# Kernel tuning notes

Measured on AMD Instinct MI355X. Metric: run time of the kernel, lower is better.

Reference implementation:

```python
import jax, jax.numpy as jnp
import numpy as np

BATCH, MAXPV = 32, 50
RULENUM, PROPNUM = 256, 256  # must be equal (eye(rulenum) * property_importance)
ENT_DIM, RULE_DIM = 128, 128
ENTITYNUM = 50000
THRESHOLD = 0.5


def _l2norm(x, eps=1e-12):
    # F.normalize(p=2, dim=-1)
    n = jnp.linalg.norm(x, axis=-1, keepdims=True)
    return x / jnp.clip(n, eps)


def setup_inputs() -> dict:
    key = jax.random.key(0)
    ks = jax.random.split(key, 20)
    d_in = ENT_DIM + RULE_DIM
    inp = {
        'property': jax.random.randint(ks[0], (BATCH, MAXPV), 0, ENTITYNUM),
        'value': jax.random.randint(ks[1], (BATCH, MAXPV), 0, ENTITYNUM),
        'samemask': jax.random.randint(ks[2], (BATCH, MAXPV), 0, 2),
        'padmask': jax.random.randint(ks[3], (BATCH, MAXPV), 0, 2),
        'rule_embedding': jax.random.normal(ks[4], (RULENUM, RULE_DIM), jnp.float32),
        'entity_table': jax.random.normal(ks[5], (ENTITYNUM, ENT_DIM), jnp.float32),
        # Linear weights stored (in, out); concat order in the original is (p_emb, rule_emb)
        'fc1_w': jax.random.normal(ks[6], (d_in, ENT_DIM), jnp.float32),
        'fc1_b': jax.random.normal(ks[7], (ENT_DIM,), jnp.float32) * 0.02,
        'fc2_w': jax.random.normal(ks[8], (d_in, ENT_DIM), jnp.float32),
        'fc2_b': jax.random.normal(ks[9], (ENT_DIM,), jnp.float32) * 0.02,
        'fc3_w': jax.random.normal(ks[10], (d_in, ENT_DIM), jnp.float32),
        'fc3_b': jax.random.normal(ks[11], (ENT_DIM,), jnp.float32) * 0.02,
        'fc4_w': jax.random.normal(ks[12], (ENT_DIM, 1), jnp.float32) * 0.05,
        'fc4_b': jax.random.normal(ks[13], (1,), jnp.float32) * 0.02,
        'fc5_w': jax.random.normal(ks[14], (ENT_DIM, 1), jnp.float32) * 0.05,
        'fc5_b': jax.random.normal(ks[15], (1,), jnp.float32) * 0.02,
        'fc6_w': jax.random.normal(ks[16], (ENT_DIM, ENT_DIM), jnp.float32) * 0.05,
        'fc6_b': jax.random.normal(ks[17], (ENT_DIM,), jnp.float32) * 0.02,
    }
    return inp


def reference(property, value, samemask, padmask, rule_embedding, entity_table,
              fc1_w, fc1_b, fc2_w, fc2_b, fc3_w, fc3_b,
              fc4_w, fc4_b, fc5_w, fc5_b, fc6_w, fc6_b):
    E = entity_table.shape[1]
    R = rule_embedding.shape[0]
    P = R  # propertynum == rulenum (required by eye() regularizer)

    p_emb = _l2norm(entity_table[property])   # (B, M, E)
    v_emb = _l2norm(entity_table[value])      # (B, M, E)
    r_emb = _l2norm(rule_embedding)           # (R, Dr)

    # cat(p, rule) -> Linear decomposed into two smaller matmuls (same math)
    def branch(w, b):
        return p_emb @ w[:E], r_emb @ w[E:] + b  # (B,M,Eo), (R,Eo)

    # s1 branch
    pa, ra = branch(fc1_w, fc1_b)
    h1 = jax.nn.relu(pa[:, None, :, :] + ra[None, :, None, :])   # (B,R,M,E)
    s1 = jax.nn.sigmoid(h1 @ fc4_w + fc4_b)[..., 0]              # (B,R,M)

    # p branch
    pb, rb = branch(fc2_w, fc2_b)
    h2 = jax.nn.relu(pb[:, None, :, :] + rb[None, :, None, :])
    p = jax.nn.sigmoid(h2 @ fc5_w + fc5_b)[..., 0]               # (B,R,M)

    # s2 branch
    pc, rc = branch(fc3_w, fc3_b)
    h3 = jax.nn.relu(pc[:, None, :, :] + rc[None, :, None, :])
    gv = _l2norm(h3 @ fc6_w + fc6_b)                             # (B,R,M,E)
    vb = v_emb[:, None, :, :]                                    # (B,1,M,E)
    denom = jnp.clip(jnp.linalg.norm(vb, axis=-1) * jnp.linalg.norm(gv, axis=-1), 1e-8)
    cos = jnp.sum(vb * gv, axis=-1) / denom
    s2 = 0.5 * cos + 0.5                                         # (B,R,M)

    score = p + (1.0 - p) * s2
    score = jnp.where(samemask[:, None, :] == 1, s1 * score, 1.0 - s1)

    # property importance K: fc1/fc4 on cat(prop_emb, rule_emb)
    prop_emb = _l2norm(entity_table[:P])                         # propertyids = arange(P)
    pi_h = jax.nn.relu((prop_emb @ fc1_w[:E])[None, :, :]
                       + (r_emb @ fc1_w[E:] + fc1_b)[:, None, :])  # (R,P,E)
    pi = jax.nn.sigmoid(pi_h @ fc4_w + fc4_b)[..., 0]            # (R,P)

    rule_mask = jnp.sum(pi * (pi > THRESHOLD), axis=-1) + 1.0    # (R,)

    score = score * padmask[:, None, :].astype(score.dtype)
    score = score * (s1 > THRESHOLD)
    score = jnp.sum(score, axis=-1) / rule_mask[None, :]          # (B,R)
    pooledscore = jnp.max(score, axis=1)                          # (B,)

    diag = jnp.eye(R, dtype=pi.dtype)
    reg = pi * diag + (1.0 - pi) * (1.0 - diag)
    reg = -jnp.log(reg + 1e-8) * (1.0 - diag + diag * R)
    reg_logits = jnp.mean(reg)
    return pooledscore, reg_logits
```

## Files before the change

kernel.cpp:

```cpp
#include <hip/hip_runtime.h>
#include <hip/hip_bf16.h>

#define BATCH 32
#define MAXPV 50
#define RN 256
#define PN 256
#define DIM 128
#define NI (BATCH*MAXPV)

typedef unsigned short u16;
typedef __attribute__((ext_vector_type(8))) short short8;
typedef __attribute__((ext_vector_type(4))) float f32x4;

__device__ float g_pa[NI*DIM], g_pb[NI*DIM], g_pc[NI*DIM];
__device__ float g_pp1[PN*DIM];
__device__ float g_raT[DIM*RN], g_rbT[DIM*RN];
__device__ float g_rmask[RN], g_regp[RN];
__device__ float g_scores[(size_t)NI*RN];
__device__ short8 g_bfrag[8][4][64];
__device__ float g_rcA[16*4*64*8];

__device__ __forceinline__ float bf2f(u16 u){ return __uint_as_float(((unsigned)u)<<16); }
__device__ __forceinline__ float LD(const void* p, size_t i, bool bf){
    return bf ? bf2f(((const u16*)p)[i]) : ((const float*)p)[i];
}
__device__ __forceinline__ int LDI(const void* p, size_t i, bool w64){
    return w64 ? (int)((const long long*)p)[i] : ((const int*)p)[i];
}
__device__ __forceinline__ short f2bf(float f){
    unsigned u = __float_as_uint(f);
    u = (u + 0x7FFFu + ((u>>16)&1u)) >> 16;
    return (short)u;
}
__device__ __forceinline__ unsigned f2bf2(float x, float y){
    float2 f; f.x=x; f.y=y;
    __hip_bfloat162 h = __float22bfloat162_rn(f);
    union { __hip_bfloat162 h; unsigned u; } c; c.h=h; return c.u;
}
__device__ __forceinline__ bool det_bf16(const void* ent){
    int l = threadIdx.x & 63;
    u16 v = ((const u16*)ent)[(size_t)2*(l*4)*977];
    int e = (v>>7)&0xFF;
    return __popcll(__ballot(e>=120 && e<=133)) >= 48;
}
__device__ __forceinline__ bool det_i64(const void* prop){
    int l = threadIdx.x & 63;
    bool z = (l<32) ? (((const unsigned*)prop)[2*l+1]==0u) : false;
    return __popcll(__ballot(z)) >= 30;
}
__device__ __forceinline__ float wred(float v){
#pragma unroll
    for(int o=32;o;o>>=1) v += __shfl_xor(v,o,64);
    return v;
}
__device__ __forceinline__ double wredd(double v){
#pragma unroll
    for(int o=32;o;o>>=1) v += __shfl_xor(v,o,64);
    return v;
}
__device__ __forceinline__ float wmax(float v){
#pragma unroll
    for(int o=32;o;o>>=1) v = fmaxf(v,__shfl_xor(v,o,64));
    return v;
}

__global__ __launch_bounds__(256) void k_pre(
    const void* __restrict__ ent, const void* __restrict__ rule,
    const void* __restrict__ prop, const void* __restrict__ fc6w,
    const void* __restrict__ fc1w, const void* __restrict__ fc2w, const void* __restrict__ fc3w,
    const void* __restrict__ fc1b, const void* __restrict__ fc2b, const void* __restrict__ fc3b){
    const bool bf = det_bf16(ent);
    const int blk = blockIdx.x, tid = threadIdx.x;
    if(blk >= 364){
        int nt = blk-364;
        int ks = tid>>6, lane = tid&63;
        int n = nt*16 + (lane&15);
        int k0 = ks*32 + (lane>>4)*8;
        short8 v;
#pragma unroll
        for(int j=0;j<8;j++) v[j] = f2bf(LD(fc6w,(size_t)(k0+j)*DIM + n, bf));
        g_bfrag[nt][ks][lane] = v;
        if(nt==0){ g_rmask[tid] = 1.f; g_regp[tid] = 0.f; }
        return;
    }
    __shared__ float s_w[64*DIM];
    __shared__ float s_in[16*DIM];
    __shared__ float s_bias[DIM];
    const void* w; size_t woff=0; const void* bptr=nullptr;
    float* out=nullptr; int row0; int mode=0; int srcsel;
    if(blk < 300){
        int wsel = blk/100; row0 = (blk%100)*16; srcsel = 0;
        w   = (wsel==0)?fc1w:(wsel==1)?fc2w:fc3w;
        out = (wsel==0)?g_pa:(wsel==1)?g_pb:g_pc;
    } else if(blk < 348){
        int rblk = blk-300; int wsel = rblk>>4; row0 = (rblk&15)*16; srcsel = 1;
        w    = (wsel==0)?fc1w:(wsel==1)?fc2w:fc3w;
        bptr = (wsel==0)?fc1b:(wsel==1)?fc2b:fc3b;
        woff = DIM*DIM; mode = wsel+1;
    } else { row0=(blk-348)*16; w=fc1w; out=g_pp1; srcsel=2; }
    const bool w64 = (srcsel==0) ? det_i64(prop) : false;
    {
        const int l = tid & 63;
        for(int it=0; it<4; it++){
            int lr = it*4 + (tid>>6);
            int row = row0 + lr;
            const void* src; size_t off;
            if(srcsel==0){ src=ent;  off=(size_t)LDI(prop,row,w64)*DIM; }
            else if(srcsel==1){ src=rule; off=(size_t)row*DIM; }
            else { src=ent; off=(size_t)row*DIM; }
            float a = LD(src,off+l,bf), b = LD(src,off+l+64,bf);
            float n = fmaxf(sqrtf((float)wredd((double)a*a+(double)b*b)), 1e-12f);
            s_in[lr*DIM+l]=a/n; s_in[lr*DIM+l+64]=b/n;
        }
    }
    if(tid<DIM) s_bias[tid] = bptr ? LD(bptr,tid,bf) : 0.f;
    const int j = tid & 127;
    const int rb8 = (tid>>7)*8;
    double acc[8] = {0,0,0,0,0,0,0,0};
    for(int half=0; half<2; half++){
        __syncthreads();
        for(int t=tid; t<64*DIM; t+=256)
            s_w[t] = LD(w, woff + (size_t)(half*64 + (t>>7))*DIM + (t&127), bf);
        __syncthreads();
        for(int k=0;k<64;k++){
            float wk = s_w[k*DIM + j];
#pragma unroll
            for(int rr=0;rr<8;rr++)
                acc[rr] += (double)s_in[(rb8+rr)*DIM + half*64 + k]*(double)wk;
        }
    }
    const double bj = (double)s_bias[j];
#pragma unroll
    for(int rr=0;rr<8;rr++){
        const int row = row0 + rb8 + rr;
        const float vv = (float)(bj + acc[rr]);
        if(mode==0)      out[(size_t)row*DIM + j] = vv;
        else if(mode==1) g_raT[j*256 + row] = vv;
        else if(mode==2) g_rbT[j*256 + row] = vv;
        else {
            int mt=row>>4, am=row&15, ks=j>>5, quad=(j>>3)&3, jj=j&7;
            g_rcA[((mt*4+ks)*64 + quad*16+am)*8 + jj] = vv;
        }
    }
}

__global__ __launch_bounds__(256) void k_score(
    const void* __restrict__ ent, const void* __restrict__ prop, const void* __restrict__ val,
    const void* __restrict__ same, const void* __restrict__ pad,
    const void* __restrict__ fc4w, const void* __restrict__ fc4b,
    const void* __restrict__ fc5w, const void* __restrict__ fc5b,
    const void* __restrict__ fc6b){
    const int blk = blockIdx.x, tid = threadIdx.x;
    const bool bf = det_bf16(ent);
    if(blk >= NI*2){
        __shared__ float s_a[4][DIM];
        __shared__ double s_pf4[DIM];
        const int i0 = (blk - NI*2)*4;
        if(tid<DIM) s_pf4[tid]=(double)LD(fc4w,tid,bf);
        for(int t=tid; t<4*DIM; t+=256){
            int ii=t>>7, k=t&127;
            s_a[ii][k] = g_pp1[(size_t)(i0+ii)*DIM+k];
        }
        __syncthreads();
        const int r = tid;
        double d[4]={0.0,0.0,0.0,0.0};
        for(int k=0;k<DIM;k++){
            float rav = g_raT[k*256+r];
            double f4k = s_pf4[k];
#pragma unroll
            for(int ii=0;ii<4;ii++)
                d[ii] += (double)fmaxf(s_a[ii][k]+rav,0.f)*f4k;
        }
        const double b4 = (double)LD(fc4b,0,bf);
        float mask_sum = 0.f, reg_sum = 0.f;
#pragma unroll
        for(int ii=0;ii<4;ii++){
            int p = i0 + ii;
            double sd = d[ii] + b4;
            float piv = 1.f/(1.f+expf(-(float)sd));
            if(sd > 0.0) mask_sum += piv;
            float eff = (p==r) ? piv : (1.f - piv);
            float wgt = (p==r) ? (float)RN : 1.f;
            reg_sum += -logf(eff + 1e-8f)*wgt;
        }
        atomicAdd(&g_rmask[r], mask_sum);
        atomicAdd(&g_regp[r], reg_sum);
        return;
    }
    const int i = blk >> 1, h = blk & 1;
    const bool w64 = det_i64(prop);
    if(LDI(pad,i,w64)!=1) return;
    const bool issame = (LDI(same,i,w64)==1);

    __shared__ float s_pa[DIM], s_pb[DIM], s_pc[DIM], s_v[DIM];
    __shared__ float s_f5[DIM];
    __shared__ double s_f4[DIM];
    __shared__ float2 s_s1p[DIM];
    __shared__ float s_st[128][4][2];

    if(tid < DIM){
        s_pa[tid] = g_pa[(size_t)i*DIM + tid];
        s_pb[tid] = g_pb[(size_t)i*DIM + tid];
        s_pc[tid] = g_pc[(size_t)i*DIM + tid];
        s_f4[tid] = (double)LD(fc4w,tid,bf);
        s_f5[tid] = LD(fc5w,tid,bf);
    } else if(tid < 192){
        const int l = tid - 128;
        size_t off = (size_t)LDI(val,i,w64)*DIM;
        float a = LD(ent,off+l,bf), b = LD(ent,off+l+64,bf);
        float n = fmaxf(sqrtf((float)wredd((double)a*a+(double)b*b)), 1e-12f);
        s_v[l]=a/n; s_v[l+64]=b/n;
    }
    __syncthreads();

    if(tid < 128){
        const int r = h*128 + tid;
        double d = 0.0; float pq = 0.f;
        if(issame){
            for(int k=0;k<DIM;k++){
                float rav = g_raT[k*256+r];
                float rbv = g_rbT[k*256+r];
                d += (double)fmaxf(s_pa[k]+rav,0.f)*s_f4[k];
                pq = fmaf(fmaxf(s_pb[k]+rbv,0.f), s_f5[k], pq);
            }
        } else {
            for(int k=0;k<DIM;k++){
                float rav = g_raT[k*256+r];
                d += (double)fmaxf(s_pa[k]+rav,0.f)*s_f4[k];
            }
        }
        const double b4 = (double)LD(fc4b,0,bf);
        double sd = d + b4;
        float s1v = 1.f/(1.f+expf(-(float)sd));
        if(issame){
            const float b5 = LD(fc5b,0,bf);
            float p = 1.f/(1.f+expf(-(pq + b5)));
            float2 o; o.x = (sd > 0.0) ? s1v : -s1v; o.y = p;
            s_s1p[tid] = o;
        } else {
            g_scores[(size_t)i*RN + r] = (sd > 0.0) ? (1.f - s1v) : 0.f;
        }
    }
    if(!issame) return;
    __syncthreads();

    const int w = tid>>6, l = tid&63;
    const int am = l&15, quad = l>>4;
    short8 bA[4], bB[4];
#pragma unroll
    for(int ks=0; ks<4; ks++){ bA[ks]=g_bfrag[2*w][ks][l]; bB[ks]=g_bfrag[2*w+1][ks][l]; }
    const int n0 = w*32 + am, n1 = n0 + 16;
    const float v0 = s_v[n0], v1 = s_v[n1];
    const float b60 = LD(fc6b, n0, bf), b61 = LD(fc6b, n1, bf);
    float vl = s_v[l], vh = s_v[l+64];
    const float nvb = sqrtf(wred(vl*vl + vh*vh));

    int mt = h*8;
    float4 c[8];
#pragma unroll
    for(int ks=0; ks<4; ks++){
        const float* rp = &g_rcA[((mt*4+ks)*64 + l)*8];
        c[2*ks]   = *(const float4*)rp;
        c[2*ks+1] = *(const float4*)(rp+4);
    }
    for(int mtl=0; mtl<8; mtl++){
        float4 n[8];
        if(mtl < 7){
#pragma unroll
            for(int ks=0; ks<4; ks++){
                const float* rp = &g_rcA[(((mt+1)*4+ks)*64 + l)*8];
                n[2*ks]   = *(const float4*)rp;
                n[2*ks+1] = *(const float4*)(rp+4);
            }
        }
        short8 a[4];
#pragma unroll
        for(int ks=0; ks<4; ks++){
            const float4 p0 = *(const float4*)&s_pc[ks*32 + quad*8];
            const float4 p1 = *(const float4*)&s_pc[ks*32 + quad*8 + 4];
            const float4 c0 = c[2*ks], c1 = c[2*ks+1];
            union { short8 s; unsigned u[4]; } t;
            t.u[0] = f2bf2(fmaxf(p0.x+c0.x,0.f), fmaxf(p0.y+c0.y,0.f));
            t.u[1] = f2bf2(fmaxf(p0.z+c0.z,0.f), fmaxf(p0.w+c0.w,0.f));
            t.u[2] = f2bf2(fmaxf(p1.x+c1.x,0.f), fmaxf(p1.y+c1.y,0.f));
            t.u[3] = f2bf2(fmaxf(p1.z+c1.z,0.f), fmaxf(p1.w+c1.w,0.f));
            a[ks] = t.s;
        }
        f32x4 acc0 = {0.f,0.f,0.f,0.f}, acc1 = {0.f,0.f,0.f,0.f};
#pragma unroll
        for(int ks=0; ks<4; ks++){
            acc0 = __builtin_amdgcn_mfma_f32_16x16x32_bf16(a[ks], bA[ks], acc0, 0,0,0);
            acc1 = __builtin_amdgcn_mfma_f32_16x16x32_bf16(a[ks], bB[ks], acc1, 0,0,0);
        }
#pragma unroll
        for(int q=0; q<4; q++){
            float x0 = acc0[q] + b60;
            float x1 = acc1[q] + b61;
            float ss = x0*x0 + x1*x1;
            float dv = x0*v0 + x1*v1;
#pragma unroll
            for(int o=1;o<16;o<<=1){ ss += __shfl_xor(ss,o,64); dv += __shfl_xor(dv,o,64); }
            if(am==0){
                int row = mtl*16 + quad*4 + q;
                s_st[row][w][0] = ss;
                s_st[row][w][1] = dv;
            }
        }
#pragma unroll
        for(int x=0;x<8;x++) c[x] = n[x];
        mt++;
    }
    __syncthreads();
    if(tid < 128){
        const int r = h*128 + tid;
        float ss = s_st[tid][0][0]+s_st[tid][1][0]+s_st[tid][2][0]+s_st[tid][3][0];
        float dv = s_st[tid][0][1]+s_st[tid][1][1]+s_st[tid][2][1]+s_st[tid][3][1];
        float2 sp = s_s1p[tid];
        float s1 = fabsf(sp.x);
        float gate = (sp.x > 0.f) ? 1.f : 0.f;
        float pp = sp.y;
        float nx = sqrtf(ss);
        float clipnx = fmaxf(nx, 1e-12f);
        float gvn = nx/clipnx;
        float denom = fmaxf(nvb*gvn, 1e-8f);
        float cosv = (dv/clipnx)/denom;
        float s2 = 0.5f*cosv + 0.5f;
        float sc = s1*(pp + (1.f-pp)*s2);
        g_scores[(size_t)i*RN + r] = sc * gate;
    }
}

__global__ void k_fin(float* __restrict__ out, const void* __restrict__ prop,
                      const void* __restrict__ same, const void* __restrict__ pad){
    const bool w64 = det_i64(prop);
    const int blk = blockIdx.x, tid = threadIdx.x;
    const int w = tid>>6, l = tid&63;
    __shared__ float s[4];
    if(blk < 32){
        __shared__ int s_pad[MAXPV];
        if(tid < MAXPV) s_pad[tid] = LDI(pad, (size_t)blk*MAXPV + tid, w64);
        __syncthreads();
        float ssum = 0.f;
        for(int pv=0; pv<MAXPV; pv++){
            if(!s_pad[pv]) continue;
            ssum += g_scores[((size_t)blk*MAXPV + pv)*RN + tid];
        }
        float sc = ssum / g_rmask[tid];
        float m = wmax(sc);
        if(l==0) s[w]=m;
        __syncthreads();
        if(tid==0) out[blk] = fmaxf(fmaxf(s[0],s[1]), fmaxf(s[2],s[3]));
    } else {
        float v = g_regp[tid];
        v = wred(v);
        if(l==0) s[w]=v;
        __syncthreads();
        if(tid==0) out[32] = (s[0]+s[1]+s[2]+s[3]) / (float)(RN*PN);
    }
}

extern "C" void kernel_launch(void* const* d_in, const int* in_sizes, int n_in,
                              void* d_out, int out_size, void* d_ws, size_t ws_size,
                              hipStream_t stream){
    int map[18]; for(int i=0;i<18;i++) map[i]=i;
    if(n_in>=18 && in_sizes[0]==6400000){
        const int a[18] = {14,17,16,13,15,0,2,1,4,3,6,5,8,7,10,9,12,11};
        for(int i=0;i<18;i++) map[i]=a[i];
    }
    const void* prop = d_in[map[0]];
    const void* val  = d_in[map[1]];
    const void* same = d_in[map[2]];
    const void* pad  = d_in[map[3]];
    const void* rule = d_in[map[4]];
    const void* ent  = d_in[map[5]];
    const void* fc1w = d_in[map[6]];
    const void* fc1b = d_in[map[7]];
    const void* fc2w = d_in[map[8]];
    const void* fc2b = d_in[map[9]];
    const void* fc3w = d_in[map[10]];
    const void* fc3b = d_in[map[11]];
    const void* fc4w = d_in[map[12]];
    const void* fc4b = d_in[map[13]];
    const void* fc5w = d_in[map[14]];
    const void* fc5b = d_in[map[15]];
    const void* fc6w = d_in[map[16]];
    const void* fc6b = d_in[map[17]];

    k_pre<<<372, 256, 0, stream>>>(ent, rule, prop, fc6w,
                                   fc1w, fc2w, fc3w, fc1b, fc2b, fc3b);
    k_score<<<NI*2+64, 256, 0, stream>>>(ent, prop, val, same, pad,
                                         fc4w, fc4b, fc5w, fc5b, fc6b);
    k_fin<<<33, 256, 0, stream>>>((float*)d_out, prop, same, pad);
}
```

Measured before the change: 203.9 us.

## Split fc4/fc5 dot products across thread halves and vectorize row-major rule loads

Rule projections are now stored row-major, so each thread reads its rule row with float4 loads instead of strided transposed scalar loads. In the score kernel, the fc4 (double) and fc5 dot products now run on separate 128-thread halves instead of serially on one half, and the MFMA fragment and bias loads are hoisted before the barrier. The importance blocks move to the start of the grid so they are scheduled first. Per-thread contiguous float4 reads across rows may coalesce worse than the old transposed layout, where neighbouring lanes read neighbouring addresses.

```diff
diff --git a/kernel.cpp b/kernel.cpp
--- a/kernel.cpp
+++ b/kernel.cpp
@@ -12,13 +12,16 @@
 typedef __attribute__((ext_vector_type(8))) short short8;
 typedef __attribute__((ext_vector_type(4))) float f32x4;
 
+#define F4C(v,c) ((c)==0?(v).x:(c)==1?(v).y:(c)==2?(v).z:(v).w)
+
 __device__ float g_pa[NI*DIM], g_pb[NI*DIM], g_pc[NI*DIM];
 __device__ float g_pp1[PN*DIM];
-__device__ float g_raT[DIM*RN], g_rbT[DIM*RN];
+__device__ __attribute__((aligned(16))) float g_ra[RN*DIM];
+__device__ __attribute__((aligned(16))) float g_rb[RN*DIM];
 __device__ float g_rmask[RN], g_regp[RN];
 __device__ float g_scores[(size_t)NI*RN];
 __device__ short8 g_bfrag[8][4][64];
-__device__ float g_rcA[16*4*64*8];
+__device__ __attribute__((aligned(16))) float g_rcA[16*4*64*8];
 
 __device__ __forceinline__ float bf2f(u16 u){ return __uint_as_float(((unsigned)u)<<16); }
 __device__ __forceinline__ float LD(const void* p, size_t i, bool bf){
@@ -135,8 +138,8 @@
         const int row = row0 + rb8 + rr;
         const float vv = (float)(bj + acc[rr]);
         if(mode==0)      out[(size_t)row*DIM + j] = vv;
-        else if(mode==1) g_raT[j*256 + row] = vv;
-        else if(mode==2) g_rbT[j*256 + row] = vv;
+        else if(mode==1) g_ra[(size_t)row*DIM + j] = vv;
+        else if(mode==2) g_rb[(size_t)row*DIM + j] = vv;
         else {
             int mt=row>>4, am=row&15, ks=j>>5, quad=(j>>3)&3, jj=j&7;
             g_rcA[((mt*4+ks)*64 + quad*16+am)*8 + jj] = vv;
@@ -151,11 +154,11 @@
     const void* __restrict__ fc5w, const void* __restrict__ fc5b,
     const void* __restrict__ fc6b){
     const int blk = blockIdx.x, tid = threadIdx.x;
-    const bool bf = det_bf16(ent);
-    if(blk >= NI*2){
+    if(blk < 64){
+        const bool bf = det_bf16(ent);
         __shared__ float s_a[4][DIM];
         __shared__ double s_pf4[DIM];
-        const int i0 = (blk - NI*2)*4;
+        const int i0 = blk*4;
         if(tid<DIM) s_pf4[tid]=(double)LD(fc4w,tid,bf);
         for(int t=tid; t<4*DIM; t+=256){
             int ii=t>>7, k=t&127;
@@ -163,13 +166,24 @@
         }
         __syncthreads();
         const int r = tid;
+        const float4* rap = (const float4*)&g_ra[(size_t)r*DIM];
         double d[4]={0.0,0.0,0.0,0.0};
-        for(int k=0;k<DIM;k++){
-            float rav = g_raT[k*256+r];
-            double f4k = s_pf4[k];
-#pragma unroll
-            for(int ii=0;ii<4;ii++)
-                d[ii] += (double)fmaxf(s_a[ii][k]+rav,0.f)*f4k;
+        for(int ch=0; ch<4; ch++){
+            float4 ra[8];
+#pragma unroll
+            for(int x=0;x<8;x++) ra[x] = rap[ch*8+x];
+#pragma unroll
+            for(int x=0;x<8;x++){
+#pragma unroll
+                for(int cc=0;cc<4;cc++){
+                    const int k = ch*32 + x*4 + cc;
+                    const float rav = F4C(ra[x],cc);
+                    const double f4k = s_pf4[k];
+#pragma unroll
+                    for(int ii=0;ii<4;ii++)
+                        d[ii] += (double)fmaxf(s_a[ii][k]+rav,0.f)*f4k;
+                }
+            }
         }
         const double b4 = (double)LD(fc4b,0,bf);
         float mask_sum = 0.f, reg_sum = 0.f;
@@ -187,15 +201,16 @@
         atomicAdd(&g_regp[r], reg_sum);
         return;
     }
-    const int i = blk >> 1, h = blk & 1;
+    const int ib = blk - 64;
+    const int i = ib >> 1, h = ib & 1;
     const bool w64 = det_i64(prop);
     if(LDI(pad,i,w64)!=1) return;
     const bool issame = (LDI(same,i,w64)==1);
-
-    __shared__ float s_pa[DIM], s_pb[DIM], s_pc[DIM], s_v[DIM];
-    __shared__ float s_f5[DIM];
+    const bool bf = det_bf16(ent);
+
+    __shared__ float s_pa[DIM], s_pb[DIM], s_pc[DIM], s_v[DIM], s_f5[DIM];
     __shared__ double s_f4[DIM];
-    __shared__ float2 s_s1p[DIM];
+    __shared__ float s_s1[128], s_p[128];
     __shared__ float s_st[128][4][2];
 
     if(tid < DIM){
@@ -213,47 +228,65 @@
     }
     __syncthreads();
 
+    const int w = tid>>6, l = tid&63;
+    const int am = l&15, quad = l>>4;
+    const int n0 = w*32 + am, n1 = n0 + 16;
+    short8 bA[4], bB[4];
+    float b60=0.f, b61=0.f, v0=0.f, v1=0.f, nvb=0.f;
+    if(issame){
+#pragma unroll
+        for(int ks=0; ks<4; ks++){ bA[ks]=g_bfrag[2*w][ks][l]; bB[ks]=g_bfrag[2*w+1][ks][l]; }
+        b60 = LD(fc6b, n0, bf); b61 = LD(fc6b, n1, bf);
+        v0 = s_v[n0]; v1 = s_v[n1];
+        { float vl = s_v[l], vh = s_v[l+64]; nvb = sqrtf(wred(vl*vl + vh*vh)); }
+    }
+
+    const int rr = tid & 127;
+    const int r = h*128 + rr;
     if(tid < 128){
-        const int r = h*128 + tid;
-        double d = 0.0; float pq = 0.f;
-        if(issame){
-            for(int k=0;k<DIM;k++){
-                float rav = g_raT[k*256+r];
-                float rbv = g_rbT[k*256+r];
-                d += (double)fmaxf(s_pa[k]+rav,0.f)*s_f4[k];
-                pq = fmaf(fmaxf(s_pb[k]+rbv,0.f), s_f5[k], pq);
-            }
-        } else {
-            for(int k=0;k<DIM;k++){
-                float rav = g_raT[k*256+r];
-                d += (double)fmaxf(s_pa[k]+rav,0.f)*s_f4[k];
+        const float4* rap = (const float4*)&g_ra[(size_t)r*DIM];
+        double d = 0.0;
+        for(int ch=0; ch<4; ch++){
+            float4 ra[8];
+#pragma unroll
+            for(int x=0;x<8;x++) ra[x] = rap[ch*8+x];
+#pragma unroll
+            for(int x=0;x<8;x++){
+#pragma unroll
+                for(int cc=0;cc<4;cc++){
+                    const int k = ch*32 + x*4 + cc;
+                    const float rav = F4C(ra[x],cc);
+                    d += (double)fmaxf(s_pa[k]+rav,0.f)*s_f4[k];
+                }
             }
         }
         const double b4 = (double)LD(fc4b,0,bf);
         double sd = d + b4;
         float s1v = 1.f/(1.f+expf(-(float)sd));
-        if(issame){
-            const float b5 = LD(fc5b,0,bf);
-            float p = 1.f/(1.f+expf(-(pq + b5)));
-            float2 o; o.x = (sd > 0.0) ? s1v : -s1v; o.y = p;
-            s_s1p[tid] = o;
-        } else {
-            g_scores[(size_t)i*RN + r] = (sd > 0.0) ? (1.f - s1v) : 0.f;
-        }
+        if(issame) s_s1[rr] = (sd > 0.0) ? s1v : -s1v;
+        else g_scores[(size_t)i*RN + r] = (sd > 0.0) ? (1.f - s1v) : 0.f;
+    } else if(issame){
+        const float4* rbp = (const float4*)&g_rb[(size_t)r*DIM];
+        float pq = 0.f;
+        for(int ch=0; ch<4; ch++){
+            float4 rb[8];
+#pragma unroll
+            for(int x=0;x<8;x++) rb[x] = rbp[ch*8+x];
+#pragma unroll
+            for(int x=0;x<8;x++){
+#pragma unroll
+                for(int cc=0;cc<4;cc++){
+                    const int k = ch*32 + x*4 + cc;
+                    const float rbv = F4C(rb[x],cc);
+                    pq = fmaf(fmaxf(s_pb[k]+rbv,0.f), s_f5[k], pq);
+                }
+            }
+        }
+        const float b5 = LD(fc5b,0,bf);
+        s_p[rr] = 1.f/(1.f+expf(-(pq + b5)));
     }
     if(!issame) return;
     __syncthreads();
-
-    const int w = tid>>6, l = tid&63;
-    const int am = l&15, quad = l>>4;
-    short8 bA[4], bB[4];
-#pragma unroll
-    for(int ks=0; ks<4; ks++){ bA[ks]=g_bfrag[2*w][ks][l]; bB[ks]=g_bfrag[2*w+1][ks][l]; }
-    const int n0 = w*32 + am, n1 = n0 + 16;
-    const float v0 = s_v[n0], v1 = s_v[n1];
-    const float b60 = LD(fc6b, n0, bf), b61 = LD(fc6b, n1, bf);
-    float vl = s_v[l], vh = s_v[l+64];
-    const float nvb = sqrtf(wred(vl*vl + vh*vh));
 
     int mt = h*8;
     float4 c[8];
@@ -312,13 +345,12 @@
     }
     __syncthreads();
     if(tid < 128){
-        const int r = h*128 + tid;
+        const int r2 = h*128 + tid;
         float ss = s_st[tid][0][0]+s_st[tid][1][0]+s_st[tid][2][0]+s_st[tid][3][0];
         float dv = s_st[tid][0][1]+s_st[tid][1][1]+s_st[tid][2][1]+s_st[tid][3][1];
-        float2 sp = s_s1p[tid];
-        float s1 = fabsf(sp.x);
-        float gate = (sp.x > 0.f) ? 1.f : 0.f;
-        float pp = sp.y;
+        float s1 = fabsf(s_s1[tid]);
+        float gate = (s_s1[tid] > 0.f) ? 1.f : 0.f;
+        float pp = s_p[tid];
         float nx = sqrtf(ss);
         float clipnx = fmaxf(nx, 1e-12f);
         float gvn = nx/clipnx;
@@ -326,7 +358,7 @@
         float cosv = (dv/clipnx)/denom;
         float s2 = 0.5f*cosv + 0.5f;
         float sc = s1*(pp + (1.f-pp)*s2);
-        g_scores[(size_t)i*RN + r] = sc * gate;
+        g_scores[(size_t)i*RN + r2] = sc * gate;
     }
 }
 
```

After: 293.7 us. +44.0%, slower.
